# Optimization experiments

Hardware: AMD Instinct MI355X
Metric: run time of the kernel (lower is better)

The kernel has to match this reference:

```python
import jax, jax.numpy as jnp
import numpy as np

N_EMBD = 1024
N_HEAD = 16
HEAD_DIM = N_EMBD // N_HEAD


def setup_inputs() -> dict:
    key = jax.random.key(0)
    ks = jax.random.split(key, 5)
    B, T, C = 2, 2048, N_EMBD
    scale = 0.02
    return {
        "x": jax.random.normal(ks[0], (B, T, C), dtype=jnp.float32),
        "w_attn": jax.random.normal(ks[1], (C, 3 * C), dtype=jnp.float32) * scale,
        "b_attn": jax.random.normal(ks[2], (3 * C,), dtype=jnp.float32) * scale,
        "w_proj": jax.random.normal(ks[3], (C, C), dtype=jnp.float32) * scale,
        "b_proj": jax.random.normal(ks[4], (C,), dtype=jnp.float32) * scale,
    }


def reference(x, w_attn, b_attn, w_proj, b_proj):
    B, T, C = x.shape
    H, D = N_HEAD, HEAD_DIM
    qkv = x @ w_attn + b_attn  # [B,T,3C]
    q, k, v = jnp.split(qkv, 3, axis=-1)
    # [B,T,C] -> [B,H,T,D]
    q = q.reshape(B, T, H, D).transpose(0, 2, 1, 3)
    k = k.reshape(B, T, H, D).transpose(0, 2, 1, 3)
    v = v.reshape(B, T, H, D).transpose(0, 2, 1, 3)
    scores = jnp.einsum("bhqd,bhkd->bhqk", q, k) / jnp.sqrt(jnp.float32(D))
    causal = jnp.tril(jnp.ones((T, T), dtype=bool))
    scores = jnp.where(causal, scores, jnp.finfo(scores.dtype).min)
    attn = jax.nn.softmax(scores, axis=-1)
    y = jnp.einsum("bhqk,bhkd->bhqd", attn, v)  # [B,H,T,D]
    y = y.transpose(0, 2, 1, 3).reshape(B, T, C)
    return y @ w_proj + b_proj
```

## Files before the change

### kernel.cpp

```cpp
#include <hip/hip_runtime.h>

typedef unsigned short u16;
typedef u16 u16x4 __attribute__((ext_vector_type(4)));
typedef u16 u16x8 __attribute__((ext_vector_type(8)));
typedef __bf16 bf16x8 __attribute__((ext_vector_type(8)));
typedef float floatx4 __attribute__((ext_vector_type(4)));

#define N_EMBD 1024
#define N_HEAD 16
#define HEAD_DIM 64
#define SEQ 2048
#define BATCH 2
#define M_ROWS (BATCH * SEQ)

typedef __attribute__((address_space(1))) const unsigned char ga_t;
typedef __attribute__((address_space(3))) unsigned char la_t;

#if __has_builtin(__builtin_amdgcn_exp2f)
#define EXP2(x) __builtin_amdgcn_exp2f(x)
#else
#define EXP2(x) exp2f(x)
#endif

__device__ __forceinline__ u16 cvt_bf16(float f) {
  return __builtin_bit_cast(u16, (__bf16)f);
}

__global__ __launch_bounds__(256) void prep(const float* __restrict__ x,
                                            u16* __restrict__ xb,
                                            const float* __restrict__ wa,
                                            const float* __restrict__ wp,
                                            u16* __restrict__ outa,
                                            u16* __restrict__ outp) {
  const int bid = blockIdx.x;
  if (bid < 2048) {
    const long i = ((long)bid * 256 + threadIdx.x) * 8;
    const float4 f0 = *(const float4*)&x[i];
    const float4 f1 = *(const float4*)&x[i + 4];
    u16x8 p;
    p[0] = cvt_bf16(f0.x); p[1] = cvt_bf16(f0.y);
    p[2] = cvt_bf16(f0.z); p[3] = cvt_bf16(f0.w);
    p[4] = cvt_bf16(f1.x); p[5] = cvt_bf16(f1.y);
    p[6] = cvt_bf16(f1.z); p[7] = cvt_bf16(f1.w);
    *(u16x8*)&xb[i] = p;
    return;
  }
  __shared__ u16 tile[32][33];
  const int t = bid - 2048;
  const int gx = t & 127;
  const int gy = t >> 7;
  const int R = N_EMBD;
  const float* in;
  u16* out;
  int C, bx;
  if (gx < 96) {
    in = wa; out = outa; C = 3 * N_EMBD; bx = gx * 32;
  } else {
    in = wp; out = outp; C = N_EMBD; bx = (gx - 96) * 32;
  }
  const int by = gy * 32;
  const int tx = threadIdx.x & 31;
  const int ty = threadIdx.x >> 5;
#pragma unroll
  for (int j = 0; j < 32; j += 8)
    tile[ty + j][tx] = cvt_bf16(in[(long)(by + ty + j) * C + bx + tx]);
  __syncthreads();
#pragma unroll
  for (int j = 0; j < 32; j += 8)
    out[(long)(bx + ty + j) * R + by + tx] = tile[tx][ty + j];
}

#define BK 32

template <int MODE>
__device__ __forceinline__ void stage128(const u16* __restrict__ A,
                                         const u16* __restrict__ Bt, int bm,
                                         int bn, int kt, int K, int tid,
                                         u16* as, u16* bs) {
  const int w = tid >> 6;
  const int l = tid & 63;
  const int lrow = l >> 2;
#pragma unroll
  for (int p = 0; p < 2; ++p) {
    const int arow = p * 64 + w * 16;
    const int row = arow + lrow;
    const int sl = (l & 3) ^ ((row >> 1) & 3);
    long gA;
    if (MODE == 0) {
      gA = (long)(bm + row) * K + kt + sl * 8;
    } else {
      const int m = bm + row;
      const int b = m >> 11, t = m & 2047;
      const int k0 = kt + sl * 8;
      const int head = k0 >> 6, dd = k0 & 63;
      gA = (((long)(b * N_HEAD + head)) * SEQ + t) * HEAD_DIM + dd;
    }
    __builtin_amdgcn_global_load_lds((ga_t*)(A + gA), (la_t*)&as[arow * BK],
                                     16, 0, 0);
    const long gB = (long)(bn + row) * K + kt + sl * 8;
    __builtin_amdgcn_global_load_lds((ga_t*)(Bt + gB), (la_t*)&bs[arow * BK],
                                     16, 0, 0);
  }
}

template <int MODE>
__global__ __launch_bounds__(256) void gemm128(
    const u16* __restrict__ A, const u16* __restrict__ Bt,
    const float* __restrict__ bias, float* __restrict__ out,
    u16* __restrict__ qo, u16* __restrict__ ko, u16* __restrict__ vo, int N,
    int K) {
  __shared__ u16 As[2][128 * BK];
  __shared__ u16 Bs[2][128 * BK];
  const int tid = threadIdx.x;

  const int nx = gridDim.x;
  const int nwg = nx * gridDim.y;
  int lin = blockIdx.y * nx + blockIdx.x;
  lin = (lin & 7) * (nwg >> 3) + (lin >> 3);
  const int bm = (lin / nx) * 128;
  const int bn = (lin % nx) * 128;

  const int w = tid >> 6;
  const int l = tid & 63;
  const int wm = (w >> 1) * 64;
  const int wn = (w & 1) * 64;
  const int m16 = l & 15;
  const int quad = l >> 4;
  const int ksw = (quad ^ ((m16 >> 1) & 3)) * 8;

  floatx4 acc[4][4];
#pragma unroll
  for (int i = 0; i < 4; ++i)
#pragma unroll
    for (int j = 0; j < 4; ++j) acc[i][j] = (floatx4){0.f, 0.f, 0.f, 0.f};

  const int nk = K / BK;
  stage128<MODE>(A, Bt, bm, bn, 0, K, tid, As[0], Bs[0]);
  __syncthreads();

  int cur = 0;
  for (int t = 0; t < nk; ++t) {
    if (t + 1 < nk)
      stage128<MODE>(A, Bt, bm, bn, (t + 1) * BK, K, tid, As[cur ^ 1],
                     Bs[cur ^ 1]);

    bf16x8 af[4], bfr[4];
#pragma unroll
    for (int i = 0; i < 4; ++i)
      af[i] = __builtin_bit_cast(
          bf16x8, *(const u16x8*)&As[cur][(wm + i * 16 + m16) * BK + ksw]);
#pragma unroll
    for (int j = 0; j < 4; ++j)
      bfr[j] = __builtin_bit_cast(
          bf16x8, *(const u16x8*)&Bs[cur][(wn + j * 16 + m16) * BK + ksw]);
#pragma unroll
    for (int i = 0; i < 4; ++i)
#pragma unroll
      for (int j = 0; j < 4; ++j)
        acc[i][j] = __builtin_amdgcn_mfma_f32_16x16x32_bf16(af[i], bfr[j],
                                                            acc[i][j], 0, 0, 0);
    __syncthreads();
    cur ^= 1;
  }

#pragma unroll
  for (int i = 0; i < 4; ++i) {
#pragma unroll
    for (int j = 0; j < 4; ++j) {
      const int col = bn + wn + j * 16 + m16;
      const float bv = bias[col];
      if (MODE == 1) {
#pragma unroll
        for (int r = 0; r < 4; ++r) {
          const int row = bm + wm + i * 16 + quad * 4 + r;
          out[(long)row * N_EMBD + col] = acc[i][j][r] + bv;
        }
      } else {
        const int which = col >> 10;
        const int cc = col & 1023;
        const int h = cc >> 6;
        const int dd = cc & 63;
        const int row0 = bm + wm + i * 16 + quad * 4;
        const int b = row0 >> 11;
        const int t0 = row0 & 2047;
        if (which == 2) {
          u16x4 pk;
#pragma unroll
          for (int r = 0; r < 4; ++r) pk[r] = cvt_bf16(acc[i][j][r] + bv);
          *(u16x4*)&vo[(((long)(b * N_HEAD + h)) * HEAD_DIM + dd) * SEQ + t0] =
              pk;
        } else {
          u16* dst = (which == 0) ? qo : ko;
#pragma unroll
          for (int r = 0; r < 4; ++r)
            dst[(((long)(b * N_HEAD + h)) * SEQ + t0 + r) * HEAD_DIM + dd] =
                cvt_bf16(acc[i][j][r] + bv);
        }
      }
    }
  }
}

#define BQ 64
#define BKV 64
#define LOG2E 1.44269504f
#define NQT (SEQ / BQ)

__device__ __forceinline__ void stage_kv(const u16* __restrict__ K,
                                         const u16* __restrict__ Vt, long bh,
                                         int kt, int tid, u16* kl, u16* vl) {
#pragma unroll
  for (int i = 0; i < 2; ++i) {
    const int p = tid + 256 * i;
    const int row = p >> 3;
    const int slot = (p & 7) ^ (row & 7);
    const int wb = (i * 256 + (tid & 192)) * 8;
    __builtin_amdgcn_global_load_lds(
        (ga_t*)&K[(bh * SEQ + kt + row) * HEAD_DIM + slot * 8], (la_t*)&kl[wb],
        16, 0, 0);
    __builtin_amdgcn_global_load_lds(
        (ga_t*)&Vt[(bh * HEAD_DIM + row) * SEQ + kt + slot * 8], (la_t*)&vl[wb],
        16, 0, 0);
  }
}

__global__ __launch_bounds__(256, 4) void flash_attn(
    u16* __restrict__ Qy, const u16* __restrict__ K,
    const u16* __restrict__ Vt) {
  const int id = blockIdx.x;
  const int r = id >> 8;
  const int c = id & 255;
  const int g = c >> 5;
  const long bh = c & 31;
  const int iq = (r == 0) ? (31 - g)
               : (r == 1) ? (16 + g)
               : (r == 2) ? (15 - g)
                          : g;
  const int tid = threadIdx.x;
  const int w = tid >> 6;
  const int l = tid & 63;
  const int m16 = l & 15;
  const int quad = l >> 4;

  __shared__ u16 Kl[2][BKV * 64];
  __shared__ u16 Vl[2][64 * BKV];
  __shared__ u16 Pl[4][16 * 64];

  const float SC = 0.125f * LOG2E;
  const int qb = iq * BQ;
  const int ntiles = iq + 1;
  const int qglob = qb + w * 16 + m16;
  const int sw = (m16 & 7) << 3;

  bf16x8 qf[2];
  {
    const u16* qrow = Qy + (bh * SEQ + qglob) * HEAD_DIM;
    qf[0] = __builtin_bit_cast(bf16x8, *(const u16x8*)&qrow[quad * 8]);
    qf[1] = __builtin_bit_cast(bf16x8, *(const u16x8*)&qrow[32 + quad * 8]);
  }

  floatx4 Oacc[4];
#pragma unroll
  for (int t = 0; t < 4; ++t) Oacc[t] = (floatx4){0.f, 0.f, 0.f, 0.f};
  float mrow = -1e30f, lsum = 0.f;

  stage_kv(K, Vt, bh, 0, tid, Kl[0], Vl[0]);
  __syncthreads();

  for (int it = 0; it < ntiles; ++it) {
    const int buf = it & 1;
    const int kt = it * BKV;
    if (it + 1 < ntiles)
      stage_kv(K, Vt, bh, kt + BKV, tid, Kl[buf ^ 1], Vl[buf ^ 1]);

    floatx4 s[4];
#pragma unroll
    for (int j = 0; j < 4; ++j) s[j] = (floatx4){0.f, 0.f, 0.f, 0.f};
#pragma unroll
    for (int j = 0; j < 4; ++j)
#pragma unroll
      for (int kk = 0; kk < 2; ++kk) {
        const bf16x8 kf = __builtin_bit_cast(
            bf16x8, *(const u16x8*)&Kl[buf][(j * 16 + m16) * 64 +
                                            ((kk * 32 + quad * 8) ^ sw)]);
        s[j] = __builtin_amdgcn_mfma_f32_16x16x32_bf16(kf, qf[kk], s[j], 0, 0,
                                                       0);
      }
    if (it == ntiles - 1) {
#pragma unroll
      for (int j = 0; j < 4; ++j) {
        const int key0 = kt + j * 16 + quad * 4;
#pragma unroll
        for (int r = 0; r < 4; ++r)
          if (key0 + r > qglob) s[j][r] = -1e30f;
      }
    }

    float t0 = fmaxf(fmaxf(s[0][0], s[0][1]), fmaxf(s[0][2], s[0][3]));
    float t1 = fmaxf(fmaxf(s[1][0], s[1][1]), fmaxf(s[1][2], s[1][3]));
    float t2 = fmaxf(fmaxf(s[2][0], s[2][1]), fmaxf(s[2][2], s[2][3]));
    float t3 = fmaxf(fmaxf(s[3][0], s[3][1]), fmaxf(s[3][2], s[3][3]));
    float tm = fmaxf(fmaxf(t0, t1), fmaxf(t2, t3));
    tm = fmaxf(tm, __shfl_xor(tm, 16, 64));
    tm = fmaxf(tm, __shfl_xor(tm, 32, 64));
    const float pm = tm * SC;
    if (!__all(pm <= mrow + 4.f)) {
      const float mn = fmaxf(mrow, pm);
      const float al = EXP2(mrow - mn);
      mrow = mn;
      lsum *= al;
#pragma unroll
      for (int t = 0; t < 4; ++t)
#pragma unroll
        for (int r = 0; r < 4; ++r) Oacc[t][r] *= al;
    }

    float ls = 0.f;
#pragma unroll
    for (int j = 0; j < 4; ++j) {
      u16x4 pk;
#pragma unroll
      for (int r = 0; r < 4; ++r) {
        const float p = EXP2(__builtin_fmaf(s[j][r], SC, -mrow));
        ls += p;
        pk[r] = cvt_bf16(p);
      }
      *(u16x4*)&Pl[w][m16 * 64 + ((j * 16 + quad * 4) ^ sw)] = pk;
    }
    lsum += ls;

    bf16x8 pf[2];
    pf[0] = __builtin_bit_cast(
        bf16x8, *(const u16x8*)&Pl[w][m16 * 64 + ((quad * 8) ^ sw)]);
    pf[1] = __builtin_bit_cast(
        bf16x8, *(const u16x8*)&Pl[w][m16 * 64 + ((32 + quad * 8) ^ sw)]);
#pragma unroll
    for (int t = 0; t < 4; ++t)
#pragma unroll
      for (int kk = 0; kk < 2; ++kk) {
        const bf16x8 vf = __builtin_bit_cast(
            bf16x8, *(const u16x8*)&Vl[buf][(t * 16 + m16) * 64 +
                                            ((kk * 32 + quad * 8) ^ sw)]);
        Oacc[t] = __builtin_amdgcn_mfma_f32_16x16x32_bf16(vf, pf[kk], Oacc[t],
                                                          0, 0, 0);
      }
    __syncthreads();
  }

  float lt = lsum;
  lt += __shfl_xor(lt, 16, 64);
  lt += __shfl_xor(lt, 32, 64);
  const float invl = 1.f / lt;
#pragma unroll
  for (int t = 0; t < 4; ++t) {
    u16x4 pk;
#pragma unroll
    for (int r = 0; r < 4; ++r) pk[r] = cvt_bf16(Oacc[t][r] * invl);
    *(u16x4*)&Qy[(bh * SEQ + qglob) * HEAD_DIM + t * 16 + quad * 4] = pk;
  }
}

extern "C" void kernel_launch(void* const* d_in, const int* in_sizes, int n_in,
                              void* d_out, int out_size, void* d_ws,
                              size_t ws_size, hipStream_t stream) {
  const float* x = (const float*)d_in[0];
  const float* w_attn = (const float*)d_in[1];
  const float* b_attn = (const float*)d_in[2];
  const float* w_proj = (const float*)d_in[3];
  const float* b_proj = (const float*)d_in[4];
  float* out = (float*)d_out;

  char* ws = (char*)d_ws;
  const size_t SZ = (size_t)BATCH * N_HEAD * SEQ * HEAD_DIM * sizeof(u16);
  u16* q = (u16*)(ws);
  u16* k = (u16*)(ws + SZ);
  u16* vT = (u16*)(ws + 2 * SZ);
  u16* wT_a = (u16*)(ws + 3 * SZ);
  u16* wT_p = (u16*)(ws + 3 * SZ + (size_t)3 * N_EMBD * N_EMBD * sizeof(u16));
  u16* xb = (u16*)(ws + 3 * SZ + (size_t)4 * N_EMBD * N_EMBD * sizeof(u16));

  prep<<<2048 + 4096, 256, 0, stream>>>(x, xb, w_attn, w_proj, wT_a, wT_p);

  gemm128<0><<<dim3(3 * N_EMBD / 128, M_ROWS / 128), 256, 0, stream>>>(
      xb, wT_a, b_attn, nullptr, q, k, vT, 3 * N_EMBD, N_EMBD);

  flash_attn<<<NQT * 32, 256, 0, stream>>>(q, k, vT);

  gemm128<1><<<dim3(N_EMBD / 128, M_ROWS / 128), 256, 0, stream>>>(
      q, wT_p, b_proj, out, nullptr, nullptr, nullptr, N_EMBD, N_EMBD);
}
```

Measured before the change: 180.3 us.

## Split attention KV range across two blocks and merge partial results

Each flash-attention block now handles a pair of complementary query tiles (a and 31-a), so every block does roughly the same amount of causal work. The KV range of each tile is split in half between two blocks, each writing an unnormalized fp32 partial output plus its running max and sum. A new merge kernel combines the two halves with log-sum-exp weights and writes bf16 into the buffer that feeds the projection GEMM. This evens out per-block work and keeps the grid size at 1024, at the cost of an extra launch and fp32 partial traffic to global memory.

Measured after the change: 183.5 us. About the same (+1.8%).

```diff
diff --git a/kernel.cpp b/kernel.cpp
--- a/kernel.cpp
+++ b/kernel.cpp
@@ -205,6 +205,7 @@
 #define BKV 64
 #define LOG2E 1.44269504f
 #define NQT (SEQ / BQ)
+#define NROWS (32 * SEQ)
 
 __device__ __forceinline__ void stage_kv(const u16* __restrict__ K,
                                          const u16* __restrict__ Vt, long bh,
@@ -225,17 +226,13 @@
 }
 
 __global__ __launch_bounds__(256, 4) void flash_attn(
-    u16* __restrict__ Qy, const u16* __restrict__ K,
-    const u16* __restrict__ Vt) {
+    const u16* __restrict__ Qy, const u16* __restrict__ K,
+    const u16* __restrict__ Vt, float* __restrict__ Opart,
+    float2* __restrict__ mlpart) {
   const int id = blockIdx.x;
-  const int r = id >> 8;
-  const int c = id & 255;
-  const int g = c >> 5;
-  const long bh = c & 31;
-  const int iq = (r == 0) ? (31 - g)
-               : (r == 1) ? (16 + g)
-               : (r == 2) ? (15 - g)
-                          : g;
+  const int a = id >> 6;
+  const int h = (id >> 5) & 1;
+  const long bh = id & 31;
   const int tid = threadIdx.x;
   const int w = tid >> 6;
   const int l = tid & 63;
@@ -247,117 +244,147 @@
   __shared__ u16 Pl[4][16 * 64];
 
   const float SC = 0.125f * LOG2E;
-  const int qb = iq * BQ;
-  const int ntiles = iq + 1;
-  const int qglob = qb + w * 16 + m16;
   const int sw = (m16 & 7) << 3;
 
-  bf16x8 qf[2];
-  {
-    const u16* qrow = Qy + (bh * SEQ + qglob) * HEAD_DIM;
-    qf[0] = __builtin_bit_cast(bf16x8, *(const u16x8*)&qrow[quad * 8]);
-    qf[1] = __builtin_bit_cast(bf16x8, *(const u16x8*)&qrow[32 + quad * 8]);
-  }
-
-  floatx4 Oacc[4];
-#pragma unroll
-  for (int t = 0; t < 4; ++t) Oacc[t] = (floatx4){0.f, 0.f, 0.f, 0.f};
-  float mrow = -1e30f, lsum = 0.f;
-
-  stage_kv(K, Vt, bh, 0, tid, Kl[0], Vl[0]);
-  __syncthreads();
-
-  for (int it = 0; it < ntiles; ++it) {
-    const int buf = it & 1;
-    const int kt = it * BKV;
-    if (it + 1 < ntiles)
-      stage_kv(K, Vt, bh, kt + BKV, tid, Kl[buf ^ 1], Vl[buf ^ 1]);
-
-    floatx4 s[4];
-#pragma unroll
-    for (int j = 0; j < 4; ++j) s[j] = (floatx4){0.f, 0.f, 0.f, 0.f};
-#pragma unroll
-    for (int j = 0; j < 4; ++j)
-#pragma unroll
-      for (int kk = 0; kk < 2; ++kk) {
-        const bf16x8 kf = __builtin_bit_cast(
-            bf16x8, *(const u16x8*)&Kl[buf][(j * 16 + m16) * 64 +
-                                            ((kk * 32 + quad * 8) ^ sw)]);
-        s[j] = __builtin_amdgcn_mfma_f32_16x16x32_bf16(kf, qf[kk], s[j], 0, 0,
-                                                       0);
-      }
-    if (it == ntiles - 1) {
-#pragma unroll
-      for (int j = 0; j < 4; ++j) {
-        const int key0 = kt + j * 16 + quad * 4;
-#pragma unroll
-        for (int r = 0; r < 4; ++r)
-          if (key0 + r > qglob) s[j][r] = -1e30f;
+  for (int ph = 0; ph < 2; ++ph) {
+    const int iq = ph ? (31 - a) : a;
+    const int na = iq + 1;
+    const int mid = (na + 1) >> 1;
+    const int s0 = h ? mid : 0;
+    const int e0 = h ? na : mid;
+    const int qglob = iq * BQ + w * 16 + m16;
+
+    bf16x8 qf[2];
+    {
+      const u16* qrow = Qy + (bh * SEQ + qglob) * HEAD_DIM;
+      qf[0] = __builtin_bit_cast(bf16x8, *(const u16x8*)&qrow[quad * 8]);
+      qf[1] = __builtin_bit_cast(bf16x8, *(const u16x8*)&qrow[32 + quad * 8]);
+    }
+
+    floatx4 Oacc[4];
+#pragma unroll
+    for (int t = 0; t < 4; ++t) Oacc[t] = (floatx4){0.f, 0.f, 0.f, 0.f};
+    float mrow = -1e30f, lsum = 0.f;
+
+    if (s0 < e0) {
+      stage_kv(K, Vt, bh, s0 * BKV, tid, Kl[0], Vl[0]);
+      __syncthreads();
+
+      for (int it = s0; it < e0; ++it) {
+        const int buf = (it - s0) & 1;
+        const int kt = it * BKV;
+        if (it + 1 < e0)
+          stage_kv(K, Vt, bh, kt + BKV, tid, Kl[buf ^ 1], Vl[buf ^ 1]);
+
+        floatx4 s[4];
+#pragma unroll
+        for (int j = 0; j < 4; ++j) s[j] = (floatx4){0.f, 0.f, 0.f, 0.f};
+#pragma unroll
+        for (int j = 0; j < 4; ++j)
+#pragma unroll
+          for (int kk = 0; kk < 2; ++kk) {
+            const bf16x8 kf = __builtin_bit_cast(
+                bf16x8, *(const u16x8*)&Kl[buf][(j * 16 + m16) * 64 +
+                                                ((kk * 32 + quad * 8) ^ sw)]);
+            s[j] = __builtin_amdgcn_mfma_f32_16x16x32_bf16(kf, qf[kk], s[j], 0,
+                                                           0, 0);
+          }
+        if (it == na - 1) {
+#pragma unroll
+          for (int j = 0; j < 4; ++j) {
+            const int key0 = kt + j * 16 + quad * 4;
+#pragma unroll
+            for (int r = 0; r < 4; ++r)
+              if (key0 + r > qglob) s[j][r] = -1e30f;
+          }
+        }
+
+        float t0 = fmaxf(fmaxf(s[0][0], s[0][1]), fmaxf(s[0][2], s[0][3]));
+        float t1 = fmaxf(fmaxf(s[1][0], s[1][1]), fmaxf(s[1][2], s[1][3]));
+        float t2 = fmaxf(fmaxf(s[2][0], s[2][1]), fmaxf(s[2][2], s[2][3]));
+        float t3 = fmaxf(fmaxf(s[3][0], s[3][1]), fmaxf(s[3][2], s[3][3]));
+        float tm = fmaxf(fmaxf(t0, t1), fmaxf(t2, t3));
+        tm = fmaxf(tm, __shfl_xor(tm, 16, 64));
+        tm = fmaxf(tm, __shfl_xor(tm, 32, 64));
+        const float pm = tm * SC;
+        if (!__all(pm <= mrow + 4.f)) {
+          const float mn = fmaxf(mrow, pm);
+          const float al = EXP2(mrow - mn);
+          mrow = mn;
+          lsum *= al;
+#pragma unroll
+          for (int t = 0; t < 4; ++t)
+#pragma unroll
+            for (int r = 0; r < 4; ++r) Oacc[t][r] *= al;
+        }
+
+        float ls = 0.f;
+#pragma unroll
+        for (int j = 0; j < 4; ++j) {
+          u16x4 pk;
+#pragma unroll
+          for (int r = 0; r < 4; ++r) {
+            const float p = EXP2(__builtin_fmaf(s[j][r], SC, -mrow));
+            ls += p;
+            pk[r] = cvt_bf16(p);
+          }
+          *(u16x4*)&Pl[w][m16 * 64 + ((j * 16 + quad * 4) ^ sw)] = pk;
+        }
+        lsum += ls;
+
+        bf16x8 pf[2];
+        pf[0] = __builtin_bit_cast(
+            bf16x8, *(const u16x8*)&Pl[w][m16 * 64 + ((quad * 8) ^ sw)]);
+        pf[1] = __builtin_bit_cast(
+            bf16x8, *(const u16x8*)&Pl[w][m16 * 64 + ((32 + quad * 8) ^ sw)]);
+#pragma unroll
+        for (int t = 0; t < 4; ++t)
+#pragma unroll
+          for (int kk = 0; kk < 2; ++kk) {
+            const bf16x8 vf = __builtin_bit_cast(
+                bf16x8, *(const u16x8*)&Vl[buf][(t * 16 + m16) * 64 +
+                                                ((kk * 32 + quad * 8) ^ sw)]);
+            Oacc[t] = __builtin_amdgcn_mfma_f32_16x16x32_bf16(vf, pf[kk],
+                                                              Oacc[t], 0, 0, 0);
+          }
+        __syncthreads();
       }
     }
 
-    float t0 = fmaxf(fmaxf(s[0][0], s[0][1]), fmaxf(s[0][2], s[0][3]));
-    float t1 = fmaxf(fmaxf(s[1][0], s[1][1]), fmaxf(s[1][2], s[1][3]));
-    float t2 = fmaxf(fmaxf(s[2][0], s[2][1]), fmaxf(s[2][2], s[2][3]));
-    float t3 = fmaxf(fmaxf(s[3][0], s[3][1]), fmaxf(s[3][2], s[3][3]));
-    float tm = fmaxf(fmaxf(t0, t1), fmaxf(t2, t3));
-    tm = fmaxf(tm, __shfl_xor(tm, 16, 64));
-    tm = fmaxf(tm, __shfl_xor(tm, 32, 64));
-    const float pm = tm * SC;
-    if (!__all(pm <= mrow + 4.f)) {
-      const float mn = fmaxf(mrow, pm);
-      const float al = EXP2(mrow - mn);
-      mrow = mn;
-      lsum *= al;
-#pragma unroll
-      for (int t = 0; t < 4; ++t)
-#pragma unroll
-        for (int r = 0; r < 4; ++r) Oacc[t][r] *= al;
-    }
-
-    float ls = 0.f;
-#pragma unroll
-    for (int j = 0; j < 4; ++j) {
-      u16x4 pk;
-#pragma unroll
-      for (int r = 0; r < 4; ++r) {
-        const float p = EXP2(__builtin_fmaf(s[j][r], SC, -mrow));
-        ls += p;
-        pk[r] = cvt_bf16(p);
-      }
-      *(u16x4*)&Pl[w][m16 * 64 + ((j * 16 + quad * 4) ^ sw)] = pk;
-    }
-    lsum += ls;
-
-    bf16x8 pf[2];
-    pf[0] = __builtin_bit_cast(
-        bf16x8, *(const u16x8*)&Pl[w][m16 * 64 + ((quad * 8) ^ sw)]);
-    pf[1] = __builtin_bit_cast(
-        bf16x8, *(const u16x8*)&Pl[w][m16 * 64 + ((32 + quad * 8) ^ sw)]);
+    float lt = lsum;
+    lt += __shfl_xor(lt, 16, 64);
+    lt += __shfl_xor(lt, 32, 64);
+    const long row = bh * SEQ + qglob;
+    float* Op = Opart + (long)h * NROWS * HEAD_DIM;
 #pragma unroll
     for (int t = 0; t < 4; ++t)
-#pragma unroll
-      for (int kk = 0; kk < 2; ++kk) {
-        const bf16x8 vf = __builtin_bit_cast(
-            bf16x8, *(const u16x8*)&Vl[buf][(t * 16 + m16) * 64 +
-                                            ((kk * 32 + quad * 8) ^ sw)]);
-        Oacc[t] = __builtin_amdgcn_mfma_f32_16x16x32_bf16(vf, pf[kk], Oacc[t],
-                                                          0, 0, 0);
-      }
-    __syncthreads();
-  }
-
-  float lt = lsum;
-  lt += __shfl_xor(lt, 16, 64);
-  lt += __shfl_xor(lt, 32, 64);
-  const float invl = 1.f / lt;
-#pragma unroll
-  for (int t = 0; t < 4; ++t) {
-    u16x4 pk;
-#pragma unroll
-    for (int r = 0; r < 4; ++r) pk[r] = cvt_bf16(Oacc[t][r] * invl);
-    *(u16x4*)&Qy[(bh * SEQ + qglob) * HEAD_DIM + t * 16 + quad * 4] = pk;
-  }
+      *(floatx4*)&Op[row * HEAD_DIM + t * 16 + quad * 4] = Oacc[t];
+    if (quad == 0) mlpart[h * NROWS + row] = make_float2(mrow, lt);
+  }
+}
+
+__global__ __launch_bounds__(256) void merge_attn(
+    const float* __restrict__ Opart, const float2* __restrict__ mlpart,
+    u16* __restrict__ Qy) {
+  const int bid = blockIdx.x;
+  const int bh = (bid & 7) | (((bid >> 10) & 3) << 3);
+  const int chunk = (bid >> 3) & 127;
+  const int r = threadIdx.x >> 4;
+  const int d0 = (threadIdx.x & 15) * 4;
+  const long row = (long)bh * SEQ + chunk * 16 + r;
+  const float2 A = mlpart[row];
+  const float2 B = mlpart[NROWS + row];
+  const float M = fmaxf(A.x, B.x);
+  const float w0 = EXP2(A.x - M), w1 = EXP2(B.x - M);
+  const float inv = 1.f / (w0 * A.y + w1 * B.y);
+  const floatx4 o0 = *(const floatx4*)&Opart[row * HEAD_DIM + d0];
+  const floatx4 o1 =
+      *(const floatx4*)&Opart[(long)NROWS * HEAD_DIM + row * HEAD_DIM + d0];
+  u16x4 pk;
+#pragma unroll
+  for (int i = 0; i < 4; ++i)
+    pk[i] = cvt_bf16((w0 * o0[i] + w1 * o1[i]) * inv);
+  *(u16x4*)&Qy[row * HEAD_DIM + d0] = pk;
 }
 
 extern "C" void kernel_launch(void* const* d_in, const int* in_sizes, int n_in,
@@ -378,13 +405,19 @@
   u16* wT_a = (u16*)(ws + 3 * SZ);
   u16* wT_p = (u16*)(ws + 3 * SZ + (size_t)3 * N_EMBD * N_EMBD * sizeof(u16));
   u16* xb = (u16*)(ws + 3 * SZ + (size_t)4 * N_EMBD * N_EMBD * sizeof(u16));
+  float* Opart = (float*)(ws + (size_t)48 * 1024 * 1024);
+  float2* mlpart =
+      (float2*)(ws + (size_t)48 * 1024 * 1024 +
+                (size_t)2 * NROWS * HEAD_DIM * sizeof(float));
 
   prep<<<2048 + 4096, 256, 0, stream>>>(x, xb, w_attn, w_proj, wT_a, wT_p);
 
   gemm128<0><<<dim3(3 * N_EMBD / 128, M_ROWS / 128), 256, 0, stream>>>(
       xb, wT_a, b_attn, nullptr, q, k, vT, 3 * N_EMBD, N_EMBD);
 
-  flash_attn<<<NQT * 32, 256, 0, stream>>>(q, k, vT);
+  flash_attn<<<1024, 256, 0, stream>>>(q, k, vT, Opart, mlpart);
+
+  merge_attn<<<4096, 256, 0, stream>>>(Opart, mlpart, q);
 
   gemm128<1><<<dim3(N_EMBD / 128, M_ROWS / 128), 256, 0, stream>>>(
       q, wT_p, b_proj, out, nullptr, nullptr, nullptr, N_EMBD, N_EMBD);
```
